# Performance work log

Measured on AMD Instinct MI355X. Metric: run time of the kernel, lower is better.

Reference implementation:

```python
import jax, jax.numpy as jnp
import numpy as np

N_NODES = 100000
N_EDGES = 3200000
D = 64
NEG_SLOPE = 0.01  # torch F.leaky_relu default


def setup_inputs() -> dict:
    key = jax.random.key(0)
    ks = jax.random.split(key, 7)
    s = 1.0 / np.sqrt(D)
    x = jax.random.normal(ks[0], (N_NODES, D), jnp.float32)
    src = jax.random.randint(ks[1], (N_EDGES,), 0, N_NODES)
    dst = jax.random.randint(ks[2], (N_EDGES,), 0, N_NODES)
    W1a = jax.random.normal(ks[3], (D, D), jnp.float32) * s
    W2a = jax.random.normal(ks[4], (D, D), jnp.float32) * s
    W1b = jax.random.normal(ks[5], (D, D), jnp.float32) * s
    W2b = jax.random.normal(ks[6], (D, D), jnp.float32) * s
    return {"x": x, "W1a": W1a, "W2a": W2a, "W1b": W1b, "W2b": W2b,
            "src": src, "dst": dst}


def _ngcf_conv(x, src, dst, norm, W1, W2):
    # message: norm_ij * (W1 x_j + W2 (x_j (*) x_i)), aggregated at dst i,
    # plus self-transform W1 x_i  (NGCF propagation rule, pre-activation)
    xs = x[src]            # [E, D] gather of neighbor feats
    xd = x[dst]            # [E, D] gather of center feats
    msg = norm[:, None] * (xs @ W1 + (xs * xd) @ W2)   # [E, D]
    agg = jax.ops.segment_sum(msg, dst, num_segments=x.shape[0])
    return x @ W1 + agg


def reference(x, W1a, W2a, W1b, W2b, src, dst):
    n = x.shape[0]
    ones = jnp.ones(src.shape[0], x.dtype)
    deg = jnp.maximum(jax.ops.segment_sum(ones, dst, num_segments=n), 1.0)
    norm = jax.lax.rsqrt(deg[src] * deg[dst])          # 1/sqrt(d_j d_i)
    h1 = jax.nn.leaky_relu(_ngcf_conv(x, src, dst, norm, W1a, W2a), NEG_SLOPE)
    h2 = jax.nn.leaky_relu(_ngcf_conv(h1, src, dst, norm, W1b, W2b), NEG_SLOPE)
    h3 = _ngcf_conv(h2, src, dst, norm, W1b, W2b)      # no activation (matches source)
    return jnp.concatenate([h1, h2, h3], axis=-1)      # [N, 3*D]
```

## Files before the change

### kernel.cpp

```cpp
#include <hip/hip_runtime.h>
#include <hip/hip_bf16.h>

#define N_NODES 100000
#define N_EDGES 3200000
#define D 64
#define NEG_SLOPE 0.01f

#define B_SHIFT 9
#define NB ((N_NODES + 511) >> B_SHIFT)
#define T_EDGES 4096
#define NBIN ((N_EDGES + T_EDGES - 1) / T_EDGES)

using bf16x8 = __attribute__((ext_vector_type(8))) short;
using f32x4  = __attribute__((ext_vector_type(4))) float;

__device__ __forceinline__ unsigned short f2bf(float f) {
    __hip_bfloat16 h = __float2bfloat16(f);
    return *reinterpret_cast<unsigned short*>(&h);
}
__device__ __forceinline__ float bflo(unsigned int u) { return __uint_as_float(u << 16); }
__device__ __forceinline__ float bfhi(unsigned int u) { return __uint_as_float(u & 0xffff0000u); }
__device__ __forceinline__ float bf2f(unsigned short h) { return __uint_as_float(((unsigned int)h) << 16); }

__global__ __launch_bounds__(256) void bhist_k(const int* __restrict__ dst, int* __restrict__ btot) {
    __shared__ int hist[NB];
    int tid = threadIdx.x;
    for (int b = tid; b < NB; b += 256) hist[b] = 0;
    __syncthreads();
    int e0 = blockIdx.x * T_EDGES;
    int e1 = min(e0 + T_EDGES, N_EDGES);
    for (int e = e0 + tid; e < e1; e += 256) atomicAdd(&hist[dst[e] >> B_SHIFT], 1);
    __syncthreads();
    for (int b = tid; b < NB; b += 256) {
        int h = hist[b];
        if (h) atomicAdd(&btot[b], h);
    }
}

__global__ __launch_bounds__(256) void bscan_k(const int* __restrict__ btot, int* __restrict__ bbase) {
    __shared__ int wsum[4];
    int t = threadIdx.x;
    int lane = t & 63, w = t >> 6;
    int v = (t < NB) ? btot[t] : 0;
    int incl = v;
    #pragma unroll
    for (int o = 1; o < 64; o <<= 1) {
        int u = __shfl_up(incl, o, 64);
        if (lane >= o) incl += u;
    }
    if (lane == 63) wsum[w] = incl;
    __syncthreads();
    int woff = 0;
    for (int k = 0; k < w; ++k) woff += wsum[k];
    if (t < NB) bbase[t] = woff + incl - v;
    if (t == NB) bbase[NB] = N_EDGES;
}

__global__ __launch_bounds__(256) void bucket_k(const int* __restrict__ src, const int* __restrict__ dst,
                                                const int* __restrict__ bbase, int* __restrict__ bcnt2,
                                                int2* __restrict__ pairs) {
    __shared__ int hist[NB];
    __shared__ int lbase[NB];
    __shared__ int lcnt[NB];
    __shared__ int gbase[NB];
    __shared__ int wsum[4];
    __shared__ int2 buf[T_EDGES];
    int tid = threadIdx.x;
    for (int b = tid; b < NB; b += 256) { hist[b] = 0; lcnt[b] = 0; }
    __syncthreads();
    int e0 = blockIdx.x * T_EDGES;
    int e1 = min(e0 + T_EDGES, N_EDGES);
    for (int e = e0 + tid; e < e1; e += 256) atomicAdd(&hist[dst[e] >> B_SHIFT], 1);
    __syncthreads();
    {
        int v = (tid < NB) ? hist[tid] : 0;
        int lane = tid & 63, w = tid >> 6;
        int incl = v;
        #pragma unroll
        for (int o = 1; o < 64; o <<= 1) {
            int u = __shfl_up(incl, o, 64);
            if (lane >= o) incl += u;
        }
        if (lane == 63) wsum[w] = incl;
        __syncthreads();
        int woff = 0;
        for (int k = 0; k < w; ++k) woff += wsum[k];
        if (tid < NB) {
            int excl = woff + incl - v;
            lbase[tid] = excl;
            int p = v ? atomicAdd(&bcnt2[tid], v) : 0;
            gbase[tid] = bbase[tid] + p - excl;
        }
    }
    __syncthreads();
    for (int e = e0 + tid; e < e1; e += 256) {
        int sv = src[e], dv = dst[e];
        int b = dv >> B_SHIFT;
        int loc = lbase[b] + atomicAdd(&lcnt[b], 1);
        buf[loc] = make_int2(sv, dv);
    }
    __syncthreads();
    int n = e1 - e0;
    for (int i = tid; i < n; i += 256) {
        int2 pr = buf[i];
        int b = pr.y >> B_SHIFT;
        pairs[gbase[b] + i] = pr;
    }
}

__global__ __launch_bounds__(512) void fine_k(const int2* __restrict__ pairs, const int* __restrict__ bbase,
                                              int* __restrict__ degi, int* __restrict__ offs,
                                              float* __restrict__ rsd, int* __restrict__ csr_src) {
    __shared__ int cnt[512];
    __shared__ int offl[512];
    __shared__ int wsum[8];
    int b = blockIdx.x, t = threadIdx.x;
    int start = bbase[b];
    int end = bbase[b + 1];
    cnt[t] = 0;
    __syncthreads();
    for (int e = start + t; e < end; e += 512) atomicAdd(&cnt[pairs[e].y & 511], 1);
    __syncthreads();
    int d = cnt[t];
    int lane = t & 63, w = t >> 6;
    int incl = d;
    #pragma unroll
    for (int o = 1; o < 64; o <<= 1) {
        int u = __shfl_up(incl, o, 64);
        if (lane >= o) incl += u;
    }
    if (lane == 63) wsum[w] = incl;
    __syncthreads();
    int woff = 0;
    for (int k = 0; k < w; ++k) woff += wsum[k];
    int myoff = start + woff + incl - d;
    offl[t] = myoff;
    int n = (b << B_SHIFT) + t;
    if (n < N_NODES) {
        degi[n] = d;
        offs[n] = myoff;
        rsd[n] = rsqrtf((float)(d > 0 ? d : 1));
    }
    cnt[t] = 0;
    __syncthreads();
    for (int e = start + t; e < end; e += 512) {
        int2 pr = pairs[e];
        int li = pr.y & 511;
        int p = atomicAdd(&cnt[li], 1);
        csr_src[offl[li] + p] = pr.x;
    }
}

__global__ __launch_bounds__(256) void cvt_k(const float* __restrict__ x, const float* __restrict__ rsd,
                                             unsigned short* __restrict__ xb) {
    int i = blockIdx.x * 256 + threadIdx.x;
    if (i < N_NODES * 16) {
        int node = i >> 4;
        float rn = rsd[node];
        float4 v = ((const float4*)x)[i];
        unsigned int lo = ((unsigned int)f2bf(rn * v.y) << 16) | f2bf(rn * v.x);
        unsigned int hi = ((unsigned int)f2bf(rn * v.w) << 16) | f2bf(rn * v.z);
        ((uint2*)xb)[i] = make_uint2(lo, hi);
    }
}

__global__ __launch_bounds__(256) void agg_k(const unsigned short* __restrict__ xb,
                                             const float* __restrict__ rsd,
                                             const int* __restrict__ offs, const int* __restrict__ degi,
                                             const int* __restrict__ csr_src, float* __restrict__ s) {
    int node = blockIdx.x * 4 + (threadIdx.x >> 6);
    if (node >= N_NODES) return;
    int lane = threadIdx.x & 63;
    int g = lane >> 3;
    int q = lane & 7;
    int start = offs[node];
    int deg = degi[node];
    const uint4* in4 = (const uint4*)xb;
    float acc0 = 0.f, acc1 = 0.f, acc2 = 0.f, acc3 = 0.f;
    float acc4 = 0.f, acc5 = 0.f, acc6 = 0.f, acc7 = 0.f;
    for (int base = 0; base < deg; base += 64) {
        int m = min(deg - base, 64);
        int idxv = csr_src[start + base + min(lane, m - 1)];
        for (int j = 0; j < m; j += 32) {
            int e0 = j + g, e1 = j + 8 + g, e2 = j + 16 + g, e3 = j + 24 + g;
            bool v0 = e0 < m, v1 = e1 < m, v2 = e2 < m, v3 = e3 < m;
            int s0 = __shfl(idxv, e0, 64);
            int s1 = __shfl(idxv, v1 ? e1 : 0, 64);
            int s2 = __shfl(idxv, v2 ? e2 : 0, 64);
            int s3 = __shfl(idxv, v3 ? e3 : 0, 64);
            uint4 p0 = in4[(size_t)s0 * 8 + q];
            uint4 p1 = in4[(size_t)s1 * 8 + q];
            uint4 p2 = in4[(size_t)s2 * 8 + q];
            uint4 p3 = in4[(size_t)s3 * 8 + q];
            float w0 = v0 ? 1.f : 0.f, w1 = v1 ? 1.f : 0.f;
            float w2 = v2 ? 1.f : 0.f, w3 = v3 ? 1.f : 0.f;
            acc0 += w0 * bflo(p0.x); acc1 += w0 * bfhi(p0.x);
            acc2 += w0 * bflo(p0.y); acc3 += w0 * bfhi(p0.y);
            acc4 += w0 * bflo(p0.z); acc5 += w0 * bfhi(p0.z);
            acc6 += w0 * bflo(p0.w); acc7 += w0 * bfhi(p0.w);
            acc0 += w1 * bflo(p1.x); acc1 += w1 * bfhi(p1.x);
            acc2 += w1 * bflo(p1.y); acc3 += w1 * bfhi(p1.y);
            acc4 += w1 * bflo(p1.z); acc5 += w1 * bfhi(p1.z);
            acc6 += w1 * bflo(p1.w); acc7 += w1 * bfhi(p1.w);
            acc0 += w2 * bflo(p2.x); acc1 += w2 * bfhi(p2.x);
            acc2 += w2 * bflo(p2.y); acc3 += w2 * bfhi(p2.y);
            acc4 += w2 * bflo(p2.z); acc5 += w2 * bfhi(p2.z);
            acc6 += w2 * bflo(p2.w); acc7 += w2 * bfhi(p2.w);
            acc0 += w3 * bflo(p3.x); acc1 += w3 * bfhi(p3.x);
            acc2 += w3 * bflo(p3.y); acc3 += w3 * bfhi(p3.y);
            acc4 += w3 * bflo(p3.z); acc5 += w3 * bfhi(p3.z);
            acc6 += w3 * bflo(p3.w); acc7 += w3 * bfhi(p3.w);
        }
    }
    #pragma unroll
    for (int off = 8; off < 64; off <<= 1) {
        acc0 += __shfl_xor(acc0, off, 64); acc1 += __shfl_xor(acc1, off, 64);
        acc2 += __shfl_xor(acc2, off, 64); acc3 += __shfl_xor(acc3, off, 64);
        acc4 += __shfl_xor(acc4, off, 64); acc5 += __shfl_xor(acc5, off, 64);
        acc6 += __shfl_xor(acc6, off, 64); acc7 += __shfl_xor(acc7, off, 64);
    }
    if (g == 0) {
        float rn = rsd[node];
        float4 r0, r1;
        r0.x = rn * acc0; r0.y = rn * acc1; r0.z = rn * acc2; r0.w = rn * acc3;
        r1.x = rn * acc4; r1.y = rn * acc5; r1.z = rn * acc6; r1.w = rn * acc7;
        ((float4*)s)[node * 16 + q * 2]     = r0;
        ((float4*)s)[node * 16 + q * 2 + 1] = r1;
    }
}

__global__ __launch_bounds__(256) void comb_k(const float* __restrict__ in, int stride,
                                              const float* __restrict__ s,
                                              const float* __restrict__ W1, const float* __restrict__ W2,
                                              float* __restrict__ out, int act,
                                              unsigned short* __restrict__ hb, const float* __restrict__ rsd,
                                              int bfout) {
    int tid = threadIdx.x;
    int w = tid >> 6;
    int l = tid & 63;
    int lr = l & 15;
    int lk = l >> 4;

    bf16x8 w1h[2], w1l[2], w2h[2], w2l[2];
    #pragma unroll
    for (int s2 = 0; s2 < 2; ++s2) {
        #pragma unroll
        for (int i = 0; i < 8; ++i) {
            int k = s2 * 32 + lk * 8 + i;
            float v1 = W1[k * D + w * 16 + lr];
            float v2 = W2[k * D + w * 16 + lr];
            unsigned short h1 = f2bf(v1);
            unsigned short h2 = f2bf(v2);
            w1h[s2][i] = (short)h1; w1l[s2][i] = (short)f2bf(v1 - bf2f(h1));
            w2h[s2][i] = (short)h2; w2l[s2][i] = (short)f2bf(v2 - bf2f(h2));
        }
    }

    int n0 = blockIdx.x * 32;
    bf16x8 ah[2][2], al[2][2], bh[2][2], bl[2][2];
    #pragma unroll
    for (int rt = 0; rt < 2; ++rt) {
        int n = n0 + rt * 16 + lr;
        const float* ip = in + (size_t)n * stride + lk * 8;
        const float* sp = s + (size_t)n * D + lk * 8;
        #pragma unroll
        for (int s2 = 0; s2 < 2; ++s2) {
            float ia[8], sa[8];
            *(float4*)&ia[0] = *(const float4*)(ip + s2 * 32);
            *(float4*)&ia[4] = *(const float4*)(ip + s2 * 32 + 4);
            *(float4*)&sa[0] = *(const float4*)(sp + s2 * 32);
            *(float4*)&sa[4] = *(const float4*)(sp + s2 * 32 + 4);
            #pragma unroll
            for (int i = 0; i < 8; ++i) {
                float a = ia[i] + sa[i];
                float b = sa[i] * ia[i];
                unsigned short hA = f2bf(a);
                unsigned short hB = f2bf(b);
                ah[rt][s2][i] = (short)hA; al[rt][s2][i] = (short)f2bf(a - bf2f(hA));
                bh[rt][s2][i] = (short)hB; bl[rt][s2][i] = (short)f2bf(b - bf2f(hB));
            }
        }
    }

    f32x4 acc[2] = {{0.f, 0.f, 0.f, 0.f}, {0.f, 0.f, 0.f, 0.f}};
    #pragma unroll
    for (int rt = 0; rt < 2; ++rt) {
        #pragma unroll
        for (int s2 = 0; s2 < 2; ++s2) {
            acc[rt] = __builtin_amdgcn_mfma_f32_16x16x32_bf16(ah[rt][s2], w1h[s2], acc[rt], 0, 0, 0);
            acc[rt] = __builtin_amdgcn_mfma_f32_16x16x32_bf16(al[rt][s2], w1h[s2], acc[rt], 0, 0, 0);
            acc[rt] = __builtin_amdgcn_mfma_f32_16x16x32_bf16(ah[rt][s2], w1l[s2], acc[rt], 0, 0, 0);
            acc[rt] = __builtin_amdgcn_mfma_f32_16x16x32_bf16(bh[rt][s2], w2h[s2], acc[rt], 0, 0, 0);
            acc[rt] = __builtin_amdgcn_mfma_f32_16x16x32_bf16(bl[rt][s2], w2h[s2], acc[rt], 0, 0, 0);
            acc[rt] = __builtin_amdgcn_mfma_f32_16x16x32_bf16(bh[rt][s2], w2l[s2], acc[rt], 0, 0, 0);
        }
    }

    #pragma unroll
    for (int rt = 0; rt < 2; ++rt) {
        #pragma unroll
        for (int r = 0; r < 4; ++r) {
            int n = n0 + rt * 16 + lk * 4 + r;
            float v = acc[rt][r];
            if (act) v = v >= 0.f ? v : NEG_SLOPE * v;
            out[(size_t)n * 192 + w * 16 + lr] = v;
            if (bfout) hb[(size_t)n * D + w * 16 + lr] = f2bf(rsd[n] * v);
        }
    }
}

extern "C" void kernel_launch(void* const* d_in, const int* in_sizes, int n_in,
                              void* d_out, int out_size, void* d_ws, size_t ws_size,
                              hipStream_t stream) {
    const float* x   = (const float*)d_in[0];
    const float* W1a = (const float*)d_in[1];
    const float* W2a = (const float*)d_in[2];
    const float* W1b = (const float*)d_in[3];
    const float* W2b = (const float*)d_in[4];
    const int*   src = (const int*)d_in[5];
    const int*   dst = (const int*)d_in[6];
    float* out = (float*)d_out;

    int*   btot    = (int*)d_ws;
    int*   bcnt2   = btot + 256;
    int*   bbase   = bcnt2 + 256;
    int*   degi    = bbase + 256;
    int*   offs    = degi + N_NODES;
    float* rsd     = (float*)(offs + N_NODES);
    int*   csr_src = (int*)(rsd + N_NODES);
    int2*  pairs   = (int2*)(csr_src + N_EDGES);
    unsigned short* xb = (unsigned short*)pairs;
    unsigned short* hb = xb + (size_t)N_NODES * D;
    float* s       = (float*)(pairs + N_EDGES);

    hipMemsetAsync(btot, 0, 512 * sizeof(int), stream);

    bhist_k<<<NBIN, 256, 0, stream>>>(dst, btot);
    bscan_k<<<1, 256, 0, stream>>>(btot, bbase);
    bucket_k<<<NBIN, 256, 0, stream>>>(src, dst, bbase, bcnt2, pairs);
    fine_k<<<NB, 512, 0, stream>>>(pairs, bbase, degi, offs, rsd, csr_src);
    cvt_k<<<(N_NODES * 16 + 255) / 256, 256, 0, stream>>>(x, rsd, xb);

    int ab = (N_NODES + 3) / 4;
    int cbg = N_NODES / 32;

    agg_k<<<ab, 256, 0, stream>>>(xb, rsd, offs, degi, csr_src, s);
    comb_k<<<cbg, 256, 0, stream>>>(x, D, s, W1a, W2a, out + 0, 1, hb, rsd, 1);
    agg_k<<<ab, 256, 0, stream>>>(hb, rsd, offs, degi, csr_src, s);
    comb_k<<<cbg, 256, 0, stream>>>(out + 0, 192, s, W1b, W2b, out + 64, 1, hb, rsd, 1);
    agg_k<<<ab, 256, 0, stream>>>(hb, rsd, offs, degi, csr_src, s);
    comb_k<<<cbg, 256, 0, stream>>>(out + 64, 192, s, W1b, W2b, out + 128, 0, hb, rsd, 0);
}
```

Measured before the change: 461.3 us.

## Pack edge pairs into 32 bits, split fine_k per half-bucket, fuse bf16 conversion

Edge pairs are packed into one 32-bit word (src<<9 | local dst), which halves the traffic of the bucket scatter and the CSR build. The write-back step now finds each element's bucket by binary search over lbase. fine_k runs two blocks per bucket, each handling half the nodes, so there is more parallelism, and it absorbs the separate cvt_k kernel by converting x to scaled bf16 from a shared rsd copy. In exchange, each pair array is read twice, with a bucket-wide count computed by both halves, and the packing relies on node indices fitting in 23 bits.

```diff
diff --git a/kernel.cpp b/kernel.cpp
--- a/kernel.cpp
+++ b/kernel.cpp
@@ -58,13 +58,13 @@
 
 __global__ __launch_bounds__(256) void bucket_k(const int* __restrict__ src, const int* __restrict__ dst,
                                                 const int* __restrict__ bbase, int* __restrict__ bcnt2,
-                                                int2* __restrict__ pairs) {
+                                                unsigned* __restrict__ pairs) {
     __shared__ int hist[NB];
     __shared__ int lbase[NB];
     __shared__ int lcnt[NB];
     __shared__ int gbase[NB];
     __shared__ int wsum[4];
-    __shared__ int2 buf[T_EDGES];
+    __shared__ unsigned buf[T_EDGES];
     int tid = threadIdx.x;
     for (int b = tid; b < NB; b += 256) { hist[b] = 0; lcnt[b] = 0; }
     __syncthreads();
@@ -97,29 +97,32 @@
         int sv = src[e], dv = dst[e];
         int b = dv >> B_SHIFT;
         int loc = lbase[b] + atomicAdd(&lcnt[b], 1);
-        buf[loc] = make_int2(sv, dv);
+        buf[loc] = ((unsigned)sv << 9) | (unsigned)(dv & 511);
     }
     __syncthreads();
     int n = e1 - e0;
     for (int i = tid; i < n; i += 256) {
-        int2 pr = buf[i];
-        int b = pr.y >> B_SHIFT;
-        pairs[gbase[b] + i] = pr;
-    }
-}
-
-__global__ __launch_bounds__(512) void fine_k(const int2* __restrict__ pairs, const int* __restrict__ bbase,
+        unsigned pr = buf[i];
+        int lo = 0, hi = NB - 1;
+        while (lo < hi) { int mid = (lo + hi + 1) >> 1; if (lbase[mid] <= i) lo = mid; else hi = mid - 1; }
+        pairs[gbase[lo] + i] = pr;
+    }
+}
+
+__global__ __launch_bounds__(512) void fine_k(const unsigned* __restrict__ pairs, const int* __restrict__ bbase,
                                               int* __restrict__ degi, int* __restrict__ offs,
-                                              float* __restrict__ rsd, int* __restrict__ csr_src) {
+                                              float* __restrict__ rsd, int* __restrict__ csr_src,
+                                              const float* __restrict__ x, unsigned short* __restrict__ xb) {
     __shared__ int cnt[512];
     __shared__ int offl[512];
     __shared__ int wsum[8];
-    int b = blockIdx.x, t = threadIdx.x;
+    __shared__ float rsdl[256];
+    int b = blockIdx.x >> 1, half = blockIdx.x & 1, t = threadIdx.x;
     int start = bbase[b];
     int end = bbase[b + 1];
     cnt[t] = 0;
     __syncthreads();
-    for (int e = start + t; e < end; e += 512) atomicAdd(&cnt[pairs[e].y & 511], 1);
+    for (int e = start + t; e < end; e += 512) atomicAdd(&cnt[pairs[e] & 511], 1);
     __syncthreads();
     int d = cnt[t];
     int lane = t & 63, w = t >> 6;
@@ -136,31 +139,37 @@
     int myoff = start + woff + incl - d;
     offl[t] = myoff;
     int n = (b << B_SHIFT) + t;
-    if (n < N_NODES) {
-        degi[n] = d;
-        offs[n] = myoff;
-        rsd[n] = rsqrtf((float)(d > 0 ? d : 1));
+    float rn = rsqrtf((float)(d > 0 ? d : 1));
+    if ((t >> 8) == half) {
+        if (n < N_NODES) {
+            degi[n] = d;
+            offs[n] = myoff;
+            rsd[n] = rn;
+        }
+        rsdl[t & 255] = rn;
     }
     cnt[t] = 0;
     __syncthreads();
     for (int e = start + t; e < end; e += 512) {
-        int2 pr = pairs[e];
-        int li = pr.y & 511;
-        int p = atomicAdd(&cnt[li], 1);
-        csr_src[offl[li] + p] = pr.x;
-    }
-}
-
-__global__ __launch_bounds__(256) void cvt_k(const float* __restrict__ x, const float* __restrict__ rsd,
-                                             unsigned short* __restrict__ xb) {
-    int i = blockIdx.x * 256 + threadIdx.x;
-    if (i < N_NODES * 16) {
-        int node = i >> 4;
-        float rn = rsd[node];
-        float4 v = ((const float4*)x)[i];
-        unsigned int lo = ((unsigned int)f2bf(rn * v.y) << 16) | f2bf(rn * v.x);
-        unsigned int hi = ((unsigned int)f2bf(rn * v.w) << 16) | f2bf(rn * v.z);
-        ((uint2*)xb)[i] = make_uint2(lo, hi);
+        unsigned pr = pairs[e];
+        int li = pr & 511;
+        if ((li >> 8) == half) {
+            int p = atomicAdd(&cnt[li], 1);
+            csr_src[offl[li] + p] = (int)(pr >> 9);
+        }
+    }
+    __syncthreads();
+    int nbase = (b << B_SHIFT) + (half << 8);
+    for (int i = t; i < 256 * 16; i += 512) {
+        int nl = i >> 4;
+        int node = nbase + nl;
+        if (node < N_NODES) {
+            float r = rsdl[nl];
+            float4 v = ((const float4*)x)[(size_t)node * 16 + (i & 15)];
+            unsigned int lo = ((unsigned int)f2bf(r * v.y) << 16) | f2bf(r * v.x);
+            unsigned int hi = ((unsigned int)f2bf(r * v.w) << 16) | f2bf(r * v.z);
+            ((uint2*)xb)[(size_t)node * 16 + (i & 15)] = make_uint2(lo, hi);
+        }
     }
 }
 
@@ -328,18 +337,17 @@
     int*   offs    = degi + N_NODES;
     float* rsd     = (float*)(offs + N_NODES);
     int*   csr_src = (int*)(rsd + N_NODES);
-    int2*  pairs   = (int2*)(csr_src + N_EDGES);
-    unsigned short* xb = (unsigned short*)pairs;
-    unsigned short* hb = xb + (size_t)N_NODES * D;
-    float* s       = (float*)(pairs + N_EDGES);
+    unsigned* pairs = (unsigned*)(csr_src + N_EDGES);
+    unsigned short* xb = (unsigned short*)(pairs + N_EDGES);
+    unsigned short* hb = (unsigned short*)pairs;
+    float* s       = (float*)(xb + (size_t)N_NODES * D);
 
     hipMemsetAsync(btot, 0, 512 * sizeof(int), stream);
 
     bhist_k<<<NBIN, 256, 0, stream>>>(dst, btot);
     bscan_k<<<1, 256, 0, stream>>>(btot, bbase);
     bucket_k<<<NBIN, 256, 0, stream>>>(src, dst, bbase, bcnt2, pairs);
-    fine_k<<<NB, 512, 0, stream>>>(pairs, bbase, degi, offs, rsd, csr_src);
-    cvt_k<<<(N_NODES * 16 + 255) / 256, 256, 0, stream>>>(x, rsd, xb);
+    fine_k<<<NB * 2, 512, 0, stream>>>(pairs, bbase, degi, offs, rsd, csr_src, x, xb);
 
     int ab = (N_NODES + 3) / 4;
     int cbg = N_NODES / 32;
```

Result: no change. 458.3 us (-0.6%).
